# Kernel optimization log

Measured on AMD Instinct MI355X. Metric: run time of the kernel, lower is better.

Reference implementation:

```python
import jax, jax.numpy as jnp
import numpy as np

EPS = 1e-3
POWER = 2


def setup_inputs() -> dict:
    key = jax.random.key(0)
    k1, k2, k3 = jax.random.split(key, 3)
    inputs = jax.random.normal(k1, (8192, 512), dtype=jnp.float32)
    keys = jax.random.normal(k2, (4096, 512), dtype=jnp.float32)
    values = jax.random.normal(k3, (4096, 1000), dtype=jnp.float32)
    return {"inputs": inputs, "keys": keys, "values": values}


def reference(inputs, keys, values):
    # x: [B, D]; keys: [P, D]; values: [P, C]
    x = inputs.reshape(inputs.shape[0], -1)
    k = keys.reshape(keys.shape[0], -1)
    sq = (
        jnp.sum(x * x, axis=1, keepdims=True)
        + jnp.sum(k * k, axis=1)[None, :]
        - 2.0 * (x @ k.T)
    )
    d = jnp.sqrt(jnp.maximum(sq, 0.0))  # torch.cdist (p=2)
    dist = EPS + d ** POWER
    attn = 1.0 / dist
    attn = attn / jnp.sum(attn, axis=1, keepdims=True)
    logits = attn @ values  # [B, C]
    return logits
```

## Files before the change

### kernel.cpp

```cpp
#include <hip/hip_runtime.h>
#include <stdint.h>

#define EPS_F 1e-3f

#define NB 8192
#define NP 4096
#define ND 512
#define NC 1000
#define NCP 1024

#define SXK 21.8966f
#define INV_SXK2 (1.0f / (SXK * SXK))
#define C2DOT (2.0f * INV_SXK2)
#define SA 72571.43f
#define INV_SA (1.0f / SA)
#define SV (127.0f / 4.7f)
#define INV_SV (4.7f / 127.0f)
#define OUTC (INV_SA * INV_SV)

typedef __attribute__((ext_vector_type(4))) int intx4;

static __device__ __forceinline__ void gl_lds16(const void* g, void* l) {
  __builtin_amdgcn_global_load_lds(
      (const __attribute__((address_space(1))) void*)g,
      (__attribute__((address_space(3))) void*)l,
      16, 0, 0);
}

static __device__ __forceinline__ signed char q8(float x, float s) {
  float v = fminf(fmaxf(x * s, -127.0f), 127.0f);
  return (signed char)__float2int_rn(v);
}


__global__ __launch_bounds__(256) void prep_kernel(
    const float* __restrict__ X, const float* __restrict__ Kk,
    const float* __restrict__ V,
    signed char* __restrict__ Xq, signed char* __restrict__ Kq,
    signed char* __restrict__ Vtq,
    float* __restrict__ xnorm, float* __restrict__ knorm,
    float* __restrict__ rowsum) {
  const int b = blockIdx.x;
  const int tid = threadIdx.x;
  __shared__ float tile[64][17];

  if (b < 3072) {
    const float* src;
    signed char* dst;
    float* nrm;
    int rbase;
    if (b < 2048) {
      src = X; dst = Xq; nrm = xnorm; rbase = b * 4;
      if (tid < 4) rowsum[b * 4 + tid] = 0.0f;
    } else {
      src = Kk; dst = Kq; nrm = knorm; rbase = (b - 2048) * 4;
    }
    const int w = tid >> 6, l = tid & 63;
    const int r = rbase + w;
    const float* p = src + (size_t)r * ND + l * 8;
    float4 v0 = *(const float4*)p;
    float4 v1 = *(const float4*)(p + 4);
    float s = v0.x * v0.x + v0.y * v0.y + v0.z * v0.z + v0.w * v0.w +
              v1.x * v1.x + v1.y * v1.y + v1.z * v1.z + v1.w * v1.w;
    union { signed char c[8]; uint2 u; } pk;
    pk.c[0] = q8(v0.x, SXK); pk.c[1] = q8(v0.y, SXK);
    pk.c[2] = q8(v0.z, SXK); pk.c[3] = q8(v0.w, SXK);
    pk.c[4] = q8(v1.x, SXK); pk.c[5] = q8(v1.y, SXK);
    pk.c[6] = q8(v1.z, SXK); pk.c[7] = q8(v1.w, SXK);
    *(uint2*)(dst + (size_t)r * ND + l * 8) = pk.u;
    for (int off = 32; off > 0; off >>= 1) s += __shfl_xor(s, off, 64);
    if (l == 0) nrm[r] = s;
  } else {
    const int t = b - 3072;
    const int pt = t & 63, ct = t >> 6;
    const int p0 = pt * 64, c0 = ct * 16;
    const int pl = tid >> 2, cf = (tid & 3) * 4;
    const float* vp = V + (size_t)(p0 + pl) * NC;
    for (int u = 0; u < 4; ++u) {
      int c = c0 + cf + u;
      tile[pl][cf + u] = (c < NC) ? vp[c] : 0.0f;
    }
    __syncthreads();
    const int cl = tid & 15, l = tid >> 4;
    const int c = c0 + cl;
    unsigned pk = 0;
    for (int u = 0; u < 4; ++u) {
      signed char bq = q8(tile[16 * u + l][cl], SV);
      pk |= ((unsigned)(unsigned char)bq) << (8 * u);
    }
    *(unsigned*)(Vtq + (size_t)c * NP + p0 + 4 * l) = pk;
  }
}

template <int KD>
static __device__ __forceinline__ void gemm_core_i8(
    const signed char* __restrict__ gA, const signed char* __restrict__ gB,
    signed char* lA, signed char* lB, intx4 (&acc)[4][4]) {
  const int tid = threadIdx.x;
  const int w = tid >> 6, lane = tid & 63;
  const int wm = w >> 1, wn = w & 1;
  const int lm = lane & 15, q = lane >> 4;
  const int frow = lane >> 3;
  const int fch = lane & 7;
  const int rsw = lm & 7;

  for (int k0 = 0; k0 < KD; k0 += 128) {
    for (int t = 0; t < 4; ++t) {
      const int row0 = w * 32 + t * 8;
      const int row = row0 + frow;
      const int lc = fch ^ (row & 7);
      gl_lds16(gA + (size_t)row * KD + k0 + lc * 16, &lA[row0 * 128]);
      gl_lds16(gB + (size_t)row * KD + k0 + lc * 16, &lB[row0 * 128]);
    }
    __syncthreads();
    for (int u = 0; u < 2; ++u) {
      intx4 af[4], bf[4];
      const int ch = ((u << 2) | q);
      for (int t = 0; t < 4; ++t) {
        const int ra = wm * 64 + t * 16 + lm;
        af[t] = *(const intx4*)&lA[ra * 128 + (ch ^ rsw) * 16];
        const int rb = wn * 64 + t * 16 + lm;
        bf[t] = *(const intx4*)&lB[rb * 128 + (ch ^ rsw) * 16];
      }
      for (int i = 0; i < 4; ++i)
        for (int j = 0; j < 4; ++j)
          acc[i][j] = __builtin_amdgcn_mfma_i32_16x16x64_i8(af[i], bf[j],
                                                            acc[i][j], 0, 0, 0);
    }
    __syncthreads();
  }
}

__global__ __launch_bounds__(256, 4) void gemm1_kernel(
    const signed char* __restrict__ A, const signed char* __restrict__ B,
    const float* __restrict__ xnorm, const float* __restrict__ knorm,
    signed char* __restrict__ attnq, float* __restrict__ rowsum) {
  __shared__ __align__(16) signed char lA[128 * 128];
  __shared__ __align__(16) signed char lB[128 * 128];
  const int tid = threadIdx.x;
  const int w = tid >> 6, lane = tid & 63;
  const int wm = w >> 1, wn = w & 1;
  const int lm = lane & 15, q = lane >> 4;
  const int bm = blockIdx.y * 128, bn = blockIdx.x * 128;

  intx4 acc[4][4];
  for (int i = 0; i < 4; ++i)
    for (int j = 0; j < 4; ++j) acc[i][j] = (intx4)(0);

  gemm_core_i8<ND>(A + (size_t)bm * ND, B + (size_t)bn * ND, lA, lB, acc);

  float kn[4];
  for (int j = 0; j < 4; ++j) kn[j] = knorm[bn + wn * 64 + j * 16 + lm];

  for (int i = 0; i < 4; ++i) {
    for (int r = 0; r < 4; ++r) {
      const int grow = bm + wm * 64 + i * 16 + q * 4 + r;
      const float xne = xnorm[grow] + EPS_F;
      float rs = 0.0f;
      unsigned pk = 0;
      for (int j = 0; j < 4; ++j) {
        float t = fmaf((float)acc[i][j][r], -C2DOT, xne + kn[j]);
        t = fmaxf(t, EPS_F);
        float a = __builtin_amdgcn_rcpf(t);
        rs += a;
        unsigned bq = (unsigned)__float2int_rn(fminf(a * SA, 127.0f));
        pk |= bq << (8 * j);
      }
      *(unsigned*)(attnq + (size_t)grow * NP + bn + wn * 64 + 4 * lm) = pk;
      rs += __shfl_xor(rs, 1, 16);
      rs += __shfl_xor(rs, 2, 16);
      rs += __shfl_xor(rs, 4, 16);
      rs += __shfl_xor(rs, 8, 16);
      if (lm == 0) atomicAdd(&rowsum[grow], rs);
    }
  }
}

__global__ __launch_bounds__(256, 4) void gemm2_kernel(
    const signed char* __restrict__ A, const signed char* __restrict__ B,
    const float* __restrict__ rowsum, float* __restrict__ out) {
  __shared__ __align__(16) signed char lA[128 * 128];
  __shared__ __align__(16) signed char lB[128 * 128];
  const int tid = threadIdx.x;
  const int w = tid >> 6, lane = tid & 63;
  const int wm = w >> 1, wn = w & 1;
  const int lm = lane & 15, q = lane >> 4;
  const int id = blockIdx.x;
  const int bn = (id >> 6) * 128;
  const int bm = (id & 63) * 128;

  intx4 acc[4][4];
  for (int i = 0; i < 4; ++i)
    for (int j = 0; j < 4; ++j) acc[i][j] = (intx4)(0);

  gemm_core_i8<NP>(A + (size_t)bm * NP, B + (size_t)bn * NP, lA, lB, acc);

  for (int i = 0; i < 4; ++i) {
    for (int r = 0; r < 4; ++r) {
      const int grow = bm + wm * 64 + i * 16 + q * 4 + r;
      const float inv = __builtin_amdgcn_rcpf(rowsum[grow]) * OUTC;
      for (int j = 0; j < 4; ++j) {
        const int gcol = bn + wn * 64 + j * 16 + lm;
        if (gcol < NC)
          out[(size_t)grow * NC + gcol] = (float)acc[i][j][r] * inv;
      }
    }
  }
}

extern "C" void kernel_launch(void* const* d_in, const int* in_sizes, int n_in,
                              void* d_out, int out_size, void* d_ws,
                              size_t ws_size, hipStream_t stream) {
  const float* X = (const float*)d_in[0];
  const float* Kk = (const float*)d_in[1];
  const float* V = (const float*)d_in[2];
  float* out = (float*)d_out;
  char* ws = (char*)d_ws;

  signed char* Xq = (signed char*)(ws + 0);
  signed char* Kq = (signed char*)(ws + 4194304);
  signed char* Vtq = (signed char*)(ws + 6291456);
  signed char* attnq = (signed char*)(ws + 10485760);
  float* xnorm = (float*)(ws + 44040192);
  float* knorm = (float*)(ws + 44072960);
  float* rowsum = (float*)(ws + 44089344);

  prep_kernel<<<7168, 256, 0, stream>>>(X, Kk, V, Xq, Kq, Vtq, xnorm, knorm,
                                        rowsum);
  gemm1_kernel<<<dim3(NP / 128, NB / 128), 256, 0, stream>>>(Xq, Kq, xnorm,
                                                             knorm, attnq,
                                                             rowsum);
  gemm2_kernel<<<512, 256, 0, stream>>>(attnq, Vtq, rowsum, out);
}
```

Measured before the change: 179.2 us.

## Double-buffer int8 GEMM LDS tiles with K=64 steps and single barrier

```diff
diff --git a/kernel.cpp b/kernel.cpp
--- a/kernel.cpp
+++ b/kernel.cpp
@@ -30,6 +30,12 @@
 static __device__ __forceinline__ signed char q8(float x, float s) {
   float v = fminf(fmaxf(x * s, -127.0f), 127.0f);
   return (signed char)__float2int_rn(v);
+}
+
+static __device__ __forceinline__ void wait_barrier() {
+  asm volatile("s_waitcnt vmcnt(0)" ::: "memory");
+  __builtin_amdgcn_s_barrier();
+  asm volatile("" ::: "memory");
 }
 
 
@@ -95,48 +101,67 @@
 template <int KD>
 static __device__ __forceinline__ void gemm_core_i8(
     const signed char* __restrict__ gA, const signed char* __restrict__ gB,
-    signed char* lA, signed char* lB, intx4 (&acc)[4][4]) {
+    signed char* lds, intx4 (&acc)[4][4]) {
   const int tid = threadIdx.x;
   const int w = tid >> 6, lane = tid & 63;
   const int wm = w >> 1, wn = w & 1;
   const int lm = lane & 15, q = lane >> 4;
-  const int frow = lane >> 3;
-  const int fch = lane & 7;
-  const int rsw = lm & 7;
-
-  for (int k0 = 0; k0 < KD; k0 += 128) {
-    for (int t = 0; t < 4; ++t) {
-      const int row0 = w * 32 + t * 8;
-      const int row = row0 + frow;
-      const int lc = fch ^ (row & 7);
-      gl_lds16(gA + (size_t)row * KD + k0 + lc * 16, &lA[row0 * 128]);
-      gl_lds16(gB + (size_t)row * KD + k0 + lc * 16, &lB[row0 * 128]);
-    }
-    __syncthreads();
-    for (int u = 0; u < 2; ++u) {
-      intx4 af[4], bf[4];
-      const int ch = ((u << 2) | q);
-      for (int t = 0; t < 4; ++t) {
-        const int ra = wm * 64 + t * 16 + lm;
-        af[t] = *(const intx4*)&lA[ra * 128 + (ch ^ rsw) * 16];
-        const int rb = wn * 64 + t * 16 + lm;
-        bf[t] = *(const intx4*)&lB[rb * 128 + (ch ^ rsw) * 16];
-      }
-      for (int i = 0; i < 4; ++i)
-        for (int j = 0; j < 4; ++j)
-          acc[i][j] = __builtin_amdgcn_mfma_i32_16x16x64_i8(af[i], bf[j],
-                                                            acc[i][j], 0, 0, 0);
-    }
-    __syncthreads();
-  }
+  const int frow = lane >> 2;
+  const int fgc = (lane & 3) ^ ((lane >> 3) & 3);
+  const int rsw = q ^ ((lm >> 1) & 3);
+  const int r0 = w * 32;
+  constexpr int NT = KD / 64;
+
+  const signed char* gAr = gA + (size_t)(r0 + frow) * KD + fgc * 16;
+  const signed char* gBr = gB + (size_t)(r0 + frow) * KD + fgc * 16;
+
+#define STAGE(kt, buf)                                                \
+  {                                                                   \
+    signed char* d = lds + (buf) * 16384 + r0 * 64;                   \
+    gl_lds16(gAr + (size_t)(kt) * 64, d);                             \
+    gl_lds16(gAr + (size_t)16 * KD + (size_t)(kt) * 64, d + 1024);    \
+    gl_lds16(gBr + (size_t)(kt) * 64, d + 8192);                      \
+    gl_lds16(gBr + (size_t)16 * KD + (size_t)(kt) * 64, d + 9216);    \
+  }
+
+#define COMPUTE(buf)                                                  \
+  {                                                                   \
+    const signed char* sA = lds + (buf) * 16384;                      \
+    const signed char* sB = sA + 8192;                                \
+    intx4 af[4], bf[4];                                               \
+    for (int i = 0; i < 4; ++i) {                                     \
+      af[i] = *(const intx4*)&sA[(wm * 64 + i * 16 + lm) * 64 +       \
+                                 rsw * 16];                           \
+      bf[i] = *(const intx4*)&sB[(wn * 64 + i * 16 + lm) * 64 +       \
+                                 rsw * 16];                           \
+    }                                                                 \
+    for (int i = 0; i < 4; ++i)                                       \
+      for (int j = 0; j < 4; ++j)                                     \
+        acc[i][j] = __builtin_amdgcn_mfma_i32_16x16x64_i8(            \
+            af[i], bf[j], acc[i][j], 0, 0, 0);                        \
+  }
+
+  STAGE(0, 0);
+  wait_barrier();
+  int cur = 0;
+#pragma unroll 2
+  for (int t = 0; t < NT - 1; ++t) {
+    STAGE(t + 1, cur ^ 1);
+    COMPUTE(cur);
+    wait_barrier();
+    cur ^= 1;
+  }
+  COMPUTE(cur);
+
+#undef STAGE
+#undef COMPUTE
 }
 
 __global__ __launch_bounds__(256, 4) void gemm1_kernel(
     const signed char* __restrict__ A, const signed char* __restrict__ B,
     const float* __restrict__ xnorm, const float* __restrict__ knorm,
     signed char* __restrict__ attnq, float* __restrict__ rowsum) {
-  __shared__ __align__(16) signed char lA[128 * 128];
-  __shared__ __align__(16) signed char lB[128 * 128];
+  __shared__ __align__(16) signed char lds[2 * 16384];
   const int tid = threadIdx.x;
   const int w = tid >> 6, lane = tid & 63;
   const int wm = w >> 1, wn = w & 1;
@@ -147,7 +172,7 @@
   for (int i = 0; i < 4; ++i)
     for (int j = 0; j < 4; ++j) acc[i][j] = (intx4)(0);
 
-  gemm_core_i8<ND>(A + (size_t)bm * ND, B + (size_t)bn * ND, lA, lB, acc);
+  gemm_core_i8<ND>(A + (size_t)bm * ND, B + (size_t)bn * ND, lds, acc);
 
   float kn[4];
   for (int j = 0; j < 4; ++j) kn[j] = knorm[bn + wn * 64 + j * 16 + lm];
@@ -179,8 +204,7 @@
 __global__ __launch_bounds__(256, 4) void gemm2_kernel(
     const signed char* __restrict__ A, const signed char* __restrict__ B,
     const float* __restrict__ rowsum, float* __restrict__ out) {
-  __shared__ __align__(16) signed char lA[128 * 128];
-  __shared__ __align__(16) signed char lB[128 * 128];
+  __shared__ __align__(16) signed char lds[2 * 16384];
   const int tid = threadIdx.x;
   const int w = tid >> 6, lane = tid & 63;
   const int wm = w >> 1, wn = w & 1;
@@ -193,7 +217,7 @@
   for (int i = 0; i < 4; ++i)
     for (int j = 0; j < 4; ++j) acc[i][j] = (intx4)(0);
 
-  gemm_core_i8<NP>(A + (size_t)bm * NP, B + (size_t)bn * NP, lA, lB, acc);
+  gemm_core_i8<NP>(A + (size_t)bm * NP, B + (size_t)bn * NP, lds, acc);
 
   for (int i = 0; i < 4; ++i) {
     for (int r = 0; r < 4; ++r) {
```

Result: slower. 189.9 us (+5.9%).

## Load MFMA operands directly from global memory instead of staging through LDS

Applied to the files above, without the earlier changes.

```diff
diff --git a/kernel.cpp b/kernel.cpp
--- a/kernel.cpp
+++ b/kernel.cpp
@@ -19,13 +19,6 @@
 #define OUTC (INV_SA * INV_SV)
 
 typedef __attribute__((ext_vector_type(4))) int intx4;
-
-static __device__ __forceinline__ void gl_lds16(const void* g, void* l) {
-  __builtin_amdgcn_global_load_lds(
-      (const __attribute__((address_space(1))) void*)g,
-      (__attribute__((address_space(3))) void*)l,
-      16, 0, 0);
-}
 
 static __device__ __forceinline__ signed char q8(float x, float s) {
   float v = fminf(fmaxf(x * s, -127.0f), 127.0f);
@@ -93,61 +86,51 @@
 }
 
 template <int KD>
-static __device__ __forceinline__ void gemm_core_i8(
+static __device__ __forceinline__ void gemm_core_direct(
     const signed char* __restrict__ gA, const signed char* __restrict__ gB,
-    signed char* lA, signed char* lB, intx4 (&acc)[4][4]) {
+    intx4 (&acc)[4][4]) {
   const int tid = threadIdx.x;
   const int w = tid >> 6, lane = tid & 63;
   const int wm = w >> 1, wn = w & 1;
   const int lm = lane & 15, q = lane >> 4;
-  const int frow = lane >> 3;
-  const int fch = lane & 7;
-  const int rsw = lm & 7;
-
-  for (int k0 = 0; k0 < KD; k0 += 128) {
-    for (int t = 0; t < 4; ++t) {
-      const int row0 = w * 32 + t * 8;
-      const int row = row0 + frow;
-      const int lc = fch ^ (row & 7);
-      gl_lds16(gA + (size_t)row * KD + k0 + lc * 16, &lA[row0 * 128]);
-      gl_lds16(gB + (size_t)row * KD + k0 + lc * 16, &lB[row0 * 128]);
-    }
-    __syncthreads();
-    for (int u = 0; u < 2; ++u) {
-      intx4 af[4], bf[4];
-      const int ch = ((u << 2) | q);
-      for (int t = 0; t < 4; ++t) {
-        const int ra = wm * 64 + t * 16 + lm;
-        af[t] = *(const intx4*)&lA[ra * 128 + (ch ^ rsw) * 16];
-        const int rb = wn * 64 + t * 16 + lm;
-        bf[t] = *(const intx4*)&lB[rb * 128 + (ch ^ rsw) * 16];
-      }
-      for (int i = 0; i < 4; ++i)
-        for (int j = 0; j < 4; ++j)
-          acc[i][j] = __builtin_amdgcn_mfma_i32_16x16x64_i8(af[i], bf[j],
-                                                            acc[i][j], 0, 0, 0);
-    }
-    __syncthreads();
-  }
-}
-
-__global__ __launch_bounds__(256, 4) void gemm1_kernel(
+
+  const signed char* pa[4];
+  const signed char* pb[4];
+  for (int i = 0; i < 4; ++i) {
+    pa[i] = gA + (size_t)(wm * 64 + i * 16 + lm) * KD + q * 16;
+    pb[i] = gB + (size_t)(wn * 64 + i * 16 + lm) * KD + q * 16;
+  }
+
+#pragma unroll
+  for (int k0 = 0; k0 < KD; k0 += 64) {
+    intx4 af[4], bf[4];
+    for (int i = 0; i < 4; ++i) af[i] = *(const intx4*)(pa[i] + k0);
+    for (int i = 0; i < 4; ++i) bf[i] = *(const intx4*)(pb[i] + k0);
+    for (int i = 0; i < 4; ++i)
+      for (int j = 0; j < 4; ++j)
+        acc[i][j] = __builtin_amdgcn_mfma_i32_16x16x64_i8(af[i], bf[j],
+                                                          acc[i][j], 0, 0, 0);
+  }
+}
+
+__global__ __launch_bounds__(256, 3) void gemm1_kernel(
     const signed char* __restrict__ A, const signed char* __restrict__ B,
     const float* __restrict__ xnorm, const float* __restrict__ knorm,
     signed char* __restrict__ attnq, float* __restrict__ rowsum) {
-  __shared__ __align__(16) signed char lA[128 * 128];
-  __shared__ __align__(16) signed char lB[128 * 128];
   const int tid = threadIdx.x;
   const int w = tid >> 6, lane = tid & 63;
   const int wm = w >> 1, wn = w & 1;
   const int lm = lane & 15, q = lane >> 4;
-  const int bm = blockIdx.y * 128, bn = blockIdx.x * 128;
+  const int id = blockIdx.x;
+  const int sw = (id & 7) * 256 + (id >> 3);
+  const int bm = (sw >> 5) * 128;
+  const int bn = (sw & 31) * 128;
 
   intx4 acc[4][4];
   for (int i = 0; i < 4; ++i)
     for (int j = 0; j < 4; ++j) acc[i][j] = (intx4)(0);
 
-  gemm_core_i8<ND>(A + (size_t)bm * ND, B + (size_t)bn * ND, lA, lB, acc);
+  gemm_core_direct<ND>(A + (size_t)bm * ND, B + (size_t)bn * ND, acc);
 
   float kn[4];
   for (int j = 0; j < 4; ++j) kn[j] = knorm[bn + wn * 64 + j * 16 + lm];
@@ -176,11 +159,9 @@
   }
 }
 
-__global__ __launch_bounds__(256, 4) void gemm2_kernel(
+__global__ __launch_bounds__(256, 3) void gemm2_kernel(
     const signed char* __restrict__ A, const signed char* __restrict__ B,
     const float* __restrict__ rowsum, float* __restrict__ out) {
-  __shared__ __align__(16) signed char lA[128 * 128];
-  __shared__ __align__(16) signed char lB[128 * 128];
   const int tid = threadIdx.x;
   const int w = tid >> 6, lane = tid & 63;
   const int wm = w >> 1, wn = w & 1;
@@ -193,7 +174,7 @@
   for (int i = 0; i < 4; ++i)
     for (int j = 0; j < 4; ++j) acc[i][j] = (intx4)(0);
 
-  gemm_core_i8<NP>(A + (size_t)bm * NP, B + (size_t)bn * NP, lA, lB, acc);
+  gemm_core_direct<NP>(A + (size_t)bm * NP, B + (size_t)bn * NP, acc);
 
   for (int i = 0; i < 4; ++i) {
     for (int r = 0; r < 4; ++r) {
@@ -227,8 +208,6 @@
 
   prep_kernel<<<7168, 256, 0, stream>>>(X, Kk, V, Xq, Kq, Vtq, xnorm, knorm,
                                         rowsum);
-  gemm1_kernel<<<dim3(NP / 128, NB / 128), 256, 0, stream>>>(Xq, Kq, xnorm,
-                                                             knorm, attnq,
-                                                             rowsum);
+  gemm1_kernel<<<2048, 256, 0, stream>>>(Xq, Kq, xnorm, knorm, attnq, rowsum);
   gemm2_kernel<<<512, 256, 0, stream>>>(attnq, Vtq, rowsum, out);
 }
```

Result: slower. 288.1 us (+60.7%).

## Rewrite gemm2 with 256x128 tiles, 4-stage LDS pipeline, 8 waves

Applied to the files above, without the earlier changes.

```diff
diff --git a/kernel.cpp b/kernel.cpp
--- a/kernel.cpp
+++ b/kernel.cpp
@@ -31,6 +31,11 @@
   float v = fminf(fmaxf(x * s, -127.0f), 127.0f);
   return (signed char)__float2int_rn(v);
 }
+
+#define WVM3 asm volatile("s_waitcnt vmcnt(3)" ::: "memory")
+#define WVM0 asm volatile("s_waitcnt vmcnt(0)" ::: "memory")
+#define LGKM0 asm volatile("s_waitcnt lgkmcnt(0)" ::: "memory")
+#define SBAR0 __builtin_amdgcn_sched_barrier(0)
 
 
 __global__ __launch_bounds__(256) void prep_kernel(
@@ -176,29 +181,101 @@
   }
 }
 
-__global__ __launch_bounds__(256, 4) void gemm2_kernel(
+__global__ __launch_bounds__(512, 2) void gemm2_kernel(
     const signed char* __restrict__ A, const signed char* __restrict__ B,
     const float* __restrict__ rowsum, float* __restrict__ out) {
-  __shared__ __align__(16) signed char lA[128 * 128];
-  __shared__ __align__(16) signed char lB[128 * 128];
+  extern __shared__ signed char lds[];
   const int tid = threadIdx.x;
   const int w = tid >> 6, lane = tid & 63;
   const int wm = w >> 1, wn = w & 1;
   const int lm = lane & 15, q = lane >> 4;
+  const int frow = lane >> 2;
+  const int fgc = (lane & 3) ^ ((lane >> 3) & 3);
+  const int rsw = q ^ ((lm >> 1) & 3);
   const int id = blockIdx.x;
-  const int bn = (id >> 6) * 128;
-  const int bm = (id & 63) * 128;
+  const int bm = (id & 31) * 256;
+  const int bn = (id >> 5) * 128;
+
+  const signed char* gAr = A + (size_t)(bm + w * 32 + frow) * NP + fgc * 16;
+  const signed char* gBr = B + (size_t)(bn + w * 16 + frow) * NP + fgc * 16;
+  const int aoff = (wm * 64 + lm) * 64 + rsw * 16;
+  const int boff = (wn * 64 + lm) * 64 + rsw * 16;
 
   intx4 acc[4][4];
+#pragma unroll
   for (int i = 0; i < 4; ++i)
+#pragma unroll
     for (int j = 0; j < 4; ++j) acc[i][j] = (intx4)(0);
 
-  gemm_core_i8<NP>(A + (size_t)bm * NP, B + (size_t)bn * NP, lA, lB, acc);
-
+#define G2_STA(KT, SB)                                                  \
+  {                                                                     \
+    signed char* d = lds + (SB) + w * 2048;                             \
+    gl_lds16(gAr + (size_t)(KT) * 64, d);                               \
+    gl_lds16(gAr + 16 * (size_t)NP + (size_t)(KT) * 64, d + 1024);      \
+  }
+#define G2_STB(KT, SB)                                                  \
+  {                                                                     \
+    signed char* d = lds + (SB) + 16384 + w * 1024;                     \
+    gl_lds16(gBr + (size_t)(KT) * 64, d);                               \
+  }
+#define G2_KT(KT, CB, SB, STG, WV)                                      \
+  {                                                                     \
+    WV;                                                                 \
+    SBAR0;                                                              \
+    __builtin_amdgcn_s_barrier();                                       \
+    SBAR0;                                                              \
+    const signed char* cA = lds + (CB);                                 \
+    const signed char* cB = lds + (CB) + 16384;                         \
+    intx4 af[2], bf[4];                                                 \
+    _Pragma("unroll") for (int i = 0; i < 2; ++i)                       \
+        af[i] = *(const intx4*)(cA + aoff + i * 1024);                  \
+    _Pragma("unroll") for (int j = 0; j < 4; ++j)                       \
+        bf[j] = *(const intx4*)(cB + boff + j * 1024);                  \
+    if (STG) G2_STA((KT) + 2, SB);                                      \
+    LGKM0;                                                              \
+    SBAR0;                                                              \
+    __builtin_amdgcn_s_setprio(1);                                      \
+    _Pragma("unroll") for (int i = 0; i < 2; ++i)                       \
+        _Pragma("unroll") for (int j = 0; j < 4; ++j)                   \
+            acc[i][j] = __builtin_amdgcn_mfma_i32_16x16x64_i8(          \
+                af[i], bf[j], acc[i][j], 0, 0, 0);                      \
+    __builtin_amdgcn_s_setprio(0);                                      \
+    _Pragma("unroll") for (int i = 0; i < 2; ++i)                       \
+        af[i] = *(const intx4*)(cA + aoff + (2 + i) * 1024);            \
+    if (STG) G2_STB((KT) + 2, SB);                                      \
+    LGKM0;                                                              \
+    SBAR0;                                                              \
+    __builtin_amdgcn_s_setprio(1);                                      \
+    _Pragma("unroll") for (int i = 0; i < 2; ++i)                       \
+        _Pragma("unroll") for (int j = 0; j < 4; ++j)                   \
+            acc[2 + i][j] = __builtin_amdgcn_mfma_i32_16x16x64_i8(      \
+                af[i], bf[j], acc[2 + i][j], 0, 0, 0);                  \
+    __builtin_amdgcn_s_setprio(0);                                      \
+  }
+
+  G2_STA(0, 0); G2_STB(0, 0);
+  G2_STA(1, 24576); G2_STB(1, 24576);
+  for (int c4 = 0; c4 < 60; c4 += 4) {
+    G2_KT(c4 + 0, 0,     49152, 1, WVM3)
+    G2_KT(c4 + 1, 24576, 73728, 1, WVM3)
+    G2_KT(c4 + 2, 49152, 0,     1, WVM3)
+    G2_KT(c4 + 3, 73728, 24576, 1, WVM3)
+  }
+  G2_KT(60, 0,     49152, 1, WVM3)
+  G2_KT(61, 24576, 73728, 1, WVM3)
+  G2_KT(62, 49152, 0,     0, WVM3)
+  G2_KT(63, 73728, 0,     0, WVM0)
+#undef G2_KT
+#undef G2_STA
+#undef G2_STB
+
+#pragma unroll
   for (int i = 0; i < 4; ++i) {
+#pragma unroll
     for (int r = 0; r < 4; ++r) {
       const int grow = bm + wm * 64 + i * 16 + q * 4 + r;
       const float inv = __builtin_amdgcn_rcpf(rowsum[grow]) * OUTC;
+#pragma unroll
       for (int j = 0; j < 4; ++j) {
         const int gcol = bn + wn * 64 + j * 16 + lm;
         if (gcol < NC)
@@ -230,5 +307,5 @@
   gemm1_kernel<<<dim3(NP / 128, NB / 128), 256, 0, stream>>>(Xq, Kq, xnorm,
                                                              knorm, attnq,
                                                              rowsum);
-  gemm2_kernel<<<512, 256, 0, stream>>>(attnq, Vtq, rowsum, out);
-}
+  gemm2_kernel<<<256, 512, 98304, stream>>>(attnq, Vtq, rowsum, out);
+}
```

After: 179.0 us. Within noise of the previous version (-0.1%).
